# Performance work log

Measured on AMD Instinct MI355X. Metric: run time of the kernel, lower is better.

Reference implementation:

```python
import jax, jax.numpy as jnp
import numpy as np

D = 256      # input_dim
H = 8        # n_heads
HD = D // H  # head_dim = 32
S = 255      # num variables
S1 = S + 1   # new_seq (CLS + vars)
B = 4


def setup_inputs() -> dict:
    key = jax.random.key(0)
    ks = jax.random.split(key, 16)
    g = lambda k, shp, s=0.05: (jax.random.normal(k, shp, dtype=jnp.float32) * s)
    inp = {
        'desc_embeddings': jax.random.normal(ks[0], (B, S, D), dtype=jnp.float32),
        'name_value_embeddings': jax.random.normal(ks[1], (B, S1, D), dtype=jnp.float32),
        # q/k/v projections (nn.Linear: y = x @ W.T + b)
        'qW': g(ks[2], (D, D)), 'qb': jnp.zeros((D,), jnp.float32),
        'kW': g(ks[3], (D, D)), 'kb': jnp.zeros((D,), jnp.float32),
        'vW': g(ks[4], (D, D)), 'vb': jnp.zeros((D,), jnp.float32),
        # edge_update MLP: Linear(2D->D), LayerNorm(D), ReLU, Linear(D->D)
        'eW1': g(ks[5], (D, 2 * D)), 'eb1': jnp.zeros((D,), jnp.float32),
        'ln_g': jnp.ones((D,), jnp.float32), 'ln_b': jnp.zeros((D,), jnp.float32),
        'eW2': g(ks[6], (D, D)), 'eb2': jnp.zeros((D,), jnp.float32),
        # attn_proj: Linear(3*head_dim -> 1)
        'aW': g(ks[7], (1, 3 * HD)), 'ab': jnp.zeros((1,), jnp.float32),
    }
    return inp


def reference(desc_embeddings, name_value_embeddings, qW, qb, kW, kb, vW, vb,
              eW1, eb1, ln_g, ln_b, eW2, eb2, aW, ab):
    nve, desc = name_value_embeddings, desc_embeddings
    b, s1, _ = nve.shape
    s = s1 - 1

    # structure mask: CLS->Var on, Var->CLS off, Var-Var fully connected (self loops kept)
    new_adj = jnp.zeros((b, s1, s1), jnp.float32)
    new_adj = new_adj.at[:, 1:, 1:].set(1.0)
    new_adj = new_adj.at[:, 0, 1:].set(1.0)

    def lin(x, W, bb):
        return x @ W.T + bb

    q = lin(nve, qW, qb).reshape(b, s1, H, HD).transpose(0, 2, 1, 3)  # [B,H,S1,HD]
    k = lin(nve, kW, kb).reshape(b, s1, H, HD).transpose(0, 2, 1, 3)
    v = lin(nve, vW, vb).reshape(b, s1, H, HD).transpose(0, 2, 1, 3)

    # pairwise edge attributes [B,S1,S1,2D]
    di = jnp.broadcast_to(desc[:, :, None, :], (b, s, s, D))
    dj = jnp.broadcast_to(desc[:, None, :, :], (b, s, s, D))
    var_edge = jnp.concatenate([di, dj], axis=-1)              # [B,S,S,2D]
    cls_edge = jnp.concatenate([desc, desc], axis=-1)          # [B,S,2D]
    ea = jnp.zeros((b, s1, s1, 2 * D), jnp.float32)
    ea = ea.at[:, 1:, 1:].set(var_edge)
    ea = ea.at[:, 0, 1:].set(cls_edge)
    ea = ea.at[:, 1:, 0].set(cls_edge)

    # edge_update MLP (edge_type == 'mlp')
    h = lin(ea, eW1, eb1)
    mu = jnp.mean(h, axis=-1, keepdims=True)
    var = jnp.var(h, axis=-1, keepdims=True)
    h = ln_g * (h - mu) / jnp.sqrt(var + 1e-5) + ln_b
    h = jax.nn.relu(h)
    e = lin(h, eW2, eb2)                                       # [B,S1,S1,D]
    e = e.reshape(b, s1, s1, H, HD).transpose(0, 3, 1, 2, 4)    # [B,H,S1,S1,HD]
    e = e * new_adj[:, None, :, :, None]

    # attn_proj(cat(q_i, k_j, e_ij)) == q_i.wq + k_j.wk + e_ij.we + bias (gat_v1, no nonlinearity)
    wq, wk, we = aW[0, :HD], aW[0, HD:2 * HD], aW[0, 2 * HD:]
    logits = (jnp.einsum('bhid,d->bhi', q, wq)[:, :, :, None]
              + jnp.einsum('bhjd,d->bhj', k, wk)[:, :, None, :]
              + jnp.einsum('bhijd,d->bhij', e, we) + ab[0])    # [B,H,S1,S1]

    logits = logits + (new_adj[:, None] == 0).astype(logits.dtype) * -1e9
    attn = jax.nn.softmax(logits, axis=-1)                      # dropout omitted (eval)
    ctx = jnp.einsum('bhij,bhjd->bhid', attn, v)
    basis_outputs = ctx.transpose(0, 2, 1, 3)                   # [B,S1,H,HD]
    return basis_outputs, attn
```

## Files before the change

### kernel.cpp

```cpp
#include <hip/hip_runtime.h>
#include <math.h>

#define S 255
#define B 4

typedef _Float16 half8 __attribute__((ext_vector_type(8)));
typedef float f32x4 __attribute__((ext_vector_type(4)));

#define WS_APJ   0
#define WS_BPJ   131072
#define WS_VTF   262144
#define WS_AP    393216
#define WS_MFG   654336
#define WS_CONST 656384
#define WS_QLOG  656392
#define WS_KLOG  664584

__device__ __forceinline__ half8 cvt8(float4 a, float4 b) {
    half8 h;
    h[0]=(_Float16)a.x; h[1]=(_Float16)a.y; h[2]=(_Float16)a.z; h[3]=(_Float16)a.w;
    h[4]=(_Float16)b.x; h[5]=(_Float16)b.y; h[6]=(_Float16)b.z; h[7]=(_Float16)b.w;
    return h;
}

__global__ __launch_bounds__(256) void k1(
    const float* __restrict__ desc, const float* __restrict__ nve,
    const float* __restrict__ qW, const float* __restrict__ qb,
    const float* __restrict__ kW, const float* __restrict__ kb,
    const float* __restrict__ vW, const float* __restrict__ vb,
    const float* __restrict__ eW1, const float* __restrict__ eb1,
    const float* __restrict__ eW2, const float* __restrict__ eb2,
    const float* __restrict__ aW, float* __restrict__ ws)
{
    const int blk = blockIdx.x;
    const int tid = threadIdx.x;
    __shared__ _Float16 Af[4096];
    __shared__ _Float16 Bf[4096];
    const int wave = tid >> 6, lane = tid & 63;
    const int m16 = lane & 15, quad = lane >> 4;
    const int sr = tid & 63, sko = (tid >> 6) * 16;
    const half8 z8 = {(_Float16)0,(_Float16)0,(_Float16)0,(_Float16)0,
                      (_Float16)0,(_Float16)0,(_Float16)0,(_Float16)0};

    if (blk < 192) {
        const float *X, *W; int M, wst, wof, jobt, sub = blk;
        if (sub < 64)       { X=nve;  W=vW;  M=1024; wst=256; wof=0;   jobt=0; }
        else if (sub < 128) { X=desc; W=eW1; M=1020; wst=512; wof=0;   jobt=1; sub-=64; }
        else                { X=desc; W=eW1; M=1020; wst=512; wof=256; jobt=2; sub-=128; }
        int mBase = (sub>>2)*64, nBase = (sub&3)*64;
        f32x4 acc[2][2] = {};
        for (int k0 = 0; k0 < 256; k0 += 64) {
            half8 xa[2], wb[2];
            int xr = mBase + sr, wr = nBase + sr;
            #pragma unroll
            for (int hh = 0; hh < 2; hh++) {
                int kk = k0 + sko + hh*8;
                if (xr < M) xa[hh] = cvt8(*(const float4*)&X[xr*256 + kk],
                                          *(const float4*)&X[xr*256 + kk + 4]);
                else xa[hh] = z8;
                wb[hh] = cvt8(*(const float4*)&W[wr*wst + wof + kk],
                              *(const float4*)&W[wr*wst + wof + kk + 4]);
            }
            __syncthreads();
            #pragma unroll
            for (int hh = 0; hh < 2; hh++) {
                int krel = sko + hh*8;
                int c = krel >> 5, q2 = (krel >> 3) & 3;
                int ld = (sr & 15) + 16*q2, rt = sr >> 4;
                *(half8*)&Af[((rt*2 + c)*64 + ld)*8] = xa[hh];
                *(half8*)&Bf[((rt*2 + c)*64 + ld)*8] = wb[hh];
            }
            __syncthreads();
            int rt0 = (wave >> 1)*2, ct0 = (wave & 1)*2;
            #pragma unroll
            for (int c = 0; c < 2; c++) {
                half8 A0 = *(const half8*)&Af[(((rt0    )*2 + c)*64 + lane)*8];
                half8 A1 = *(const half8*)&Af[(((rt0 + 1)*2 + c)*64 + lane)*8];
                half8 B0 = *(const half8*)&Bf[(((ct0    )*2 + c)*64 + lane)*8];
                half8 B1 = *(const half8*)&Bf[(((ct0 + 1)*2 + c)*64 + lane)*8];
                acc[0][0] = __builtin_amdgcn_mfma_f32_16x16x32_f16(A0, B0, acc[0][0], 0,0,0);
                acc[0][1] = __builtin_amdgcn_mfma_f32_16x16x32_f16(A0, B1, acc[0][1], 0,0,0);
                acc[1][0] = __builtin_amdgcn_mfma_f32_16x16x32_f16(A1, B0, acc[1][0], 0,0,0);
                acc[1][1] = __builtin_amdgcn_mfma_f32_16x16x32_f16(A1, B1, acc[1][1], 0,0,0);
            }
        }
        int rt0 = (wave >> 1)*2, ct0 = (wave & 1)*2;
        if (jobt == 0) {
            _Float16* vtf = (_Float16*)(ws + WS_VTF);
            #pragma unroll
            for (int ci = 0; ci < 2; ci++) {
                int col = nBase + (ct0 + ci)*16 + m16;
                float bv = vb[col];
                int ct = col >> 4, n = col & 15;
                #pragma unroll
                for (int ri = 0; ri < 2; ri++)
                    #pragma unroll
                    for (int r = 0; r < 4; r++) {
                        int rr = mBase + (rt0 + ri)*16 + quad*4 + r;
                        int bb = rr >> 8, j = rr & 255;
                        int js = j >> 5, qv = (j >> 3) & 3, ev = j & 7;
                        float o = acc[ri][ci][r] + bv;
                        vtf[bb*65536 + (((ct*8 + js)*64 + n + 16*qv) << 3) + ev] = (_Float16)o;
                    }
            }
        } else {
            _Float16* OJ = (_Float16*)(ws + ((jobt == 1) ? WS_APJ : WS_BPJ));
            #pragma unroll
            for (int ci = 0; ci < 2; ci++) {
                int col = nBase + (ct0 + ci)*16 + m16;
                float bv = (jobt == 1) ? eb1[col] : 0.f;
                int ks = col >> 5, q = (col >> 3) & 3, e = col & 7;
                #pragma unroll
                for (int ri = 0; ri < 2; ri++)
                    #pragma unroll
                    for (int r = 0; r < 4; r++) {
                        int rr = mBase + (rt0 + ri)*16 + quad*4 + r;
                        if (rr < 1020) {
                            float o = acc[ri][ci][r] + bv;
                            int bb = rr / 255;
                            int j = rr - bb*255 + 1;
                            int jt = j >> 4, mm = j & 15;
                            OJ[bb*65536 + (((jt*8 + ks)*64 + mm + 16*q) << 3) + e] = (_Float16)o;
                            if (jobt == 1) ws[WS_AP + rr*256 + col] = o;
                        }
                    }
            }
        }
    } else if (blk < 208) {
        {
            int d = tid;
            float f[16] = {0,0,0,0,0,0,0,0,0,0,0,0,0,0,0,0};
            for (int hd = 0; hd < 32; hd++) {
                float wq = aW[hd], wk = aW[32+hd];
                #pragma unroll
                for (int h = 0; h < 8; h++) {
                    f[h]   = fmaf(wq, qW[(h*32+hd)*256 + d], f[h]);
                    f[8+h] = fmaf(wk, kW[(h*32+hd)*256 + d], f[8+h]);
                }
            }
            int ksd = d >> 5, q2 = (d >> 3) & 3, jj = d & 7;
            #pragma unroll
            for (int n = 0; n < 16; n++)
                Bf[((ksd*64 + n + 16*q2))*8 + jj] = (_Float16)f[n];
        }
        __syncthreads();
        int mBase = (blk - 192)*64;
        f32x4 acc = {0.f,0.f,0.f,0.f};
        for (int k0 = 0; k0 < 256; k0 += 64) {
            half8 xa[2];
            #pragma unroll
            for (int hh = 0; hh < 2; hh++) {
                int kk = k0 + sko + hh*8;
                xa[hh] = cvt8(*(const float4*)&nve[(mBase + sr)*256 + kk],
                              *(const float4*)&nve[(mBase + sr)*256 + kk + 4]);
            }
            __syncthreads();
            #pragma unroll
            for (int hh = 0; hh < 2; hh++) {
                int krel = sko + hh*8;
                int c = krel >> 5, q2 = (krel >> 3) & 3;
                int ld = (sr & 15) + 16*q2, rt = sr >> 4;
                *(half8*)&Af[((rt*2 + c)*64 + ld)*8] = xa[hh];
            }
            __syncthreads();
            #pragma unroll
            for (int c = 0; c < 2; c++) {
                half8 A  = *(const half8*)&Af[((wave*2 + c)*64 + lane)*8];
                half8 Bv = *(const half8*)&Bf[(((k0 >> 5) + c)*64 + lane)*8];
                acc = __builtin_amdgcn_mfma_f32_16x16x32_f16(A, Bv, acc, 0,0,0);
            }
        }
        #pragma unroll
        for (int r = 0; r < 4; r++) {
            int rr = mBase + wave*16 + quad*4 + r;
            int bb = rr >> 8, tt2 = rr & 255;
            if (m16 < 8) ws[WS_QLOG + (bb*8 + m16)*256 + tt2] = acc[r];
            else         ws[WS_KLOG + (bb*8 + m16 - 8)*256 + tt2] = acc[r];
        }
    } else {
        _Float16* mfg = (_Float16*)(ws + WS_MFG);
        int k = tid;
        float a8[8] = {0,0,0,0,0,0,0,0};
        for (int hd = 0; hd < 32; hd++) {
            float we = aW[64+hd];
            #pragma unroll
            for (int h = 0; h < 8; h++)
                a8[h] = fmaf(we, eW2[(h*32+hd)*256 + k], a8[h]);
        }
        int ksd = k >> 5, q2 = (k >> 3) & 3, jj = k & 7;
        #pragma unroll
        for (int h = 0; h < 8; h++)
            mfg[((ksd*64 + h + 16*q2))*8 + jj] = (_Float16)a8[h];
        #pragma unroll
        for (int n = 8; n < 16; n++)
            mfg[((ksd*64 + n + 16*q2))*8 + jj] = (_Float16)0.f;
        {
            _Float16* apj = (_Float16*)(ws + WS_APJ);
            _Float16* bpj = (_Float16*)(ws + WS_BPJ);
            int ks0 = tid >> 5, qz = (tid >> 3) & 3, ez = tid & 7;
            int ad = ((ks0*64 + 16*qz) << 3) + ez;
            #pragma unroll
            for (int bb = 0; bb < 4; bb++) {
                apj[bb*65536 + ad] = (_Float16)0.f;
                bpj[bb*65536 + ad] = (_Float16)0.f;
            }
        }
        if (tid == 0) {
            #pragma unroll
            for (int h = 0; h < 8; h++) {
                float c = 0.f;
                for (int hd = 0; hd < 32; hd++) {
                    c = fmaf(aW[64+hd], eb2[h*32+hd], c);
                    c = fmaf(aW[hd],    qb [h*32+hd], c);
                    c = fmaf(aW[32+hd], kb [h*32+hd], c);
                }
                ws[WS_CONST + h] = c;
            }
        }
    }
}

#define PLS 272

__global__ __launch_bounds__(256, 4) void k3(
    const float* __restrict__ ln_g, const float* __restrict__ ln_b,
    const float* __restrict__ ab, const float* __restrict__ ws,
    float* __restrict__ out)
{
    int b = blockIdx.y, i = blockIdx.x;
    int tid = threadIdx.x;
    __shared__ float klds[2048];
    __shared__ float PL[8*PLS];
    __shared__ float gL[256], bL[256], aL[256];
    __shared__ float2 st[256];
    __shared__ float stG[256], stSB[256], stQB[256], stSA[256], stQA[256];
    __shared__ float baseh[8], mxs[8], sms[8], saqa[8];

    int wave = tid >> 6, lane = tid & 63;
    int m16 = lane & 15, quad = lane >> 4;
    const half8 z8 = {(_Float16)0,(_Float16)0,(_Float16)0,(_Float16)0,
                      (_Float16)0,(_Float16)0,(_Float16)0,(_Float16)0};
    half8 ones8;
    #pragma unroll
    for (int e = 0; e < 8; e++) ones8[e] = (_Float16)1.0f;

    #pragma unroll
    for (int t = 0; t < 8; t++)
        klds[tid + t*256] = ws[WS_KLOG + b*2048 + tid + t*256];
    gL[tid] = ln_g[tid];
    bL[tid] = ln_b[tid];
    float av = (i >= 1) ? ws[WS_AP + ((size_t)(b*S + i - 1))*256 + tid] : 0.f;
    aL[tid] = av;
    {
        float s1 = av, s2 = av*av;
        #pragma unroll
        for (int off = 32; off >= 1; off >>= 1) {
            s1 += __shfl_xor(s1, off, 64);
            s2 += __shfl_xor(s2, off, 64);
        }
        if (lane == 0) { saqa[wave] = s1; saqa[4+wave] = s2; }
    }
    if (tid < 8)
        baseh[tid] = ws[WS_QLOG + (b*8+tid)*256 + i] + ab[0] + ws[WS_CONST + tid];
    __syncthreads();

    const _Float16* mfg = (const _Float16*)(ws + WS_MFG);
    const _Float16* bpj = (const _Float16*)(ws + WS_BPJ) + b*65536;
    const _Float16* apj = (const _Float16*)(ws + WS_APJ) + b*65536;
    const _Float16* vtf = (const _Float16*)(ws + WS_VTF) + b*65536;

    if (i >= 1) {
        #pragma unroll
        for (int tl4 = 0; tl4 < 4; tl4++) {
            int tl = wave*4 + tl4;
            f32x4 accGS = {}, accQB = {};
            #pragma unroll
            for (int ks = 0; ks < 8; ks++) {
                half8 bb = *(const half8*)&bpj[((tl*8+ks)*64 + lane) << 3];
                half8 ags;
                if (m16 == 0)
                    ags = cvt8(*(const float4*)&aL[ks*32 + quad*8],
                               *(const float4*)&aL[ks*32 + quad*8 + 4]);
                else if (m16 == 1) ags = ones8;
                else ags = z8;
                accGS = __builtin_amdgcn_mfma_f32_16x16x32_f16(ags, bb, accGS, 0,0,0);
                accQB = __builtin_amdgcn_mfma_f32_16x16x32_f16(bb,  bb, accQB, 0,0,0);
            }
            int j = tl*16 + m16;
            if (quad == 0) { stG[j] = accGS[0]; stSB[j] = accGS[1]; }
            if (quad == (m16 >> 2)) stQB[j] = accQB[m16 & 3];
        }
    } else {
        #pragma unroll
        for (int tl4 = 0; tl4 < 4; tl4++) {
            int tl = wave*4 + tl4;
            f32x4 accSB = {}, accSA = {}, accG = {}, accQA = {}, accQB = {};
            #pragma unroll
            for (int ks = 0; ks < 8; ks++) {
                int idx = ((tl*8+ks)*64 + lane) << 3;
                half8 bb = *(const half8*)&bpj[idx];
                half8 aa = *(const half8*)&apj[idx];
                half8 a1 = (m16 == 0) ? ones8 : z8;
                accSB = __builtin_amdgcn_mfma_f32_16x16x32_f16(a1, bb, accSB, 0,0,0);
                accSA = __builtin_amdgcn_mfma_f32_16x16x32_f16(a1, aa, accSA, 0,0,0);
                accG  = __builtin_amdgcn_mfma_f32_16x16x32_f16(aa, bb, accG,  0,0,0);
                accQA = __builtin_amdgcn_mfma_f32_16x16x32_f16(aa, aa, accQA, 0,0,0);
                accQB = __builtin_amdgcn_mfma_f32_16x16x32_f16(bb, bb, accQB, 0,0,0);
            }
            int j = tl*16 + m16;
            if (quad == 0) { stSB[j] = accSB[0]; stSA[j] = accSA[0]; }
            if (quad == (m16 >> 2)) {
                int r = m16 & 3;
                stG[j] = accG[r]; stQA[j] = accQA[r]; stQB[j] = accQB[r];
            }
        }
    }
    __syncthreads();

    {
        int j = tid;
        float2 v; v.x = 0.f; v.y = 0.f;
        if (j >= 1) {
            float sa, qa;
            if (i >= 1) {
                sa = saqa[0] + saqa[1] + saqa[2] + saqa[3];
                qa = saqa[4] + saqa[5] + saqa[6] + saqa[7];
            } else {
                sa = stSA[j]; qa = stQA[j];
            }
            float sb = stSB[j], qb2 = stQB[j], g = stG[j];
            float mu  = (sa + sb) * (1.0f/256.0f);
            float var = (qa + qb2 + 2.f*g) * (1.0f/256.0f) - mu*mu;
            float inv = rsqrtf(var + 1e-5f);
            v.x = inv; v.y = -mu*inv;
        }
        st[j] = v;
    }
    __syncthreads();

    f32x4 acc[4] = {};
    float2 sv[4];
    #pragma unroll
    for (int tt = 0; tt < 4; tt++)
        sv[tt] = st[(wave*4 + tt)*16 + m16];

    if (i >= 1) {
        #pragma unroll
        for (int ks = 0; ks < 8; ks++) {
            int k = ks*32 + quad*8;
            float4 a0 = *(const float4*)&aL[k], a1 = *(const float4*)&aL[k+4];
            float4 g0 = *(const float4*)&gL[k], g1 = *(const float4*)&gL[k+4];
            float4 b0 = *(const float4*)&bL[k], b1 = *(const float4*)&bL[k+4];
            half8 bf = *(const half8*)&mfg[(ks*64 + lane) << 3];
            float aa[8] = {a0.x,a0.y,a0.z,a0.w,a1.x,a1.y,a1.z,a1.w};
            float ga[8] = {g0.x,g0.y,g0.z,g0.w,g1.x,g1.y,g1.z,g1.w};
            float be[8] = {b0.x,b0.y,b0.z,b0.w,b1.x,b1.y,b1.z,b1.w};
            #pragma unroll
            for (int tt = 0; tt < 4; tt++) {
                half8 bp = *(const half8*)&bpj[(((wave*4 + tt)*8 + ks)*64 + lane) << 3];
                half8 af;
                #pragma unroll
                for (int e = 0; e < 8; e++) {
                    float c = (float)bp[e] + aa[e];
                    float w = fmaf(fmaf(c, sv[tt].x, sv[tt].y), ga[e], be[e]);
                    af[e] = (_Float16)fmaxf(w, 0.f);
                }
                acc[tt] = __builtin_amdgcn_mfma_f32_16x16x32_f16(af, bf, acc[tt], 0,0,0);
            }
        }
    } else {
        #pragma unroll
        for (int ks = 0; ks < 8; ks++) {
            int k = ks*32 + quad*8;
            float4 g0 = *(const float4*)&gL[k], g1 = *(const float4*)&gL[k+4];
            float4 b0 = *(const float4*)&bL[k], b1 = *(const float4*)&bL[k+4];
            half8 bf = *(const half8*)&mfg[(ks*64 + lane) << 3];
            float ga[8] = {g0.x,g0.y,g0.z,g0.w,g1.x,g1.y,g1.z,g1.w};
            float be[8] = {b0.x,b0.y,b0.z,b0.w,b1.x,b1.y,b1.z,b1.w};
            #pragma unroll
            for (int tt = 0; tt < 4; tt++) {
                int idx = ((((wave*4 + tt)*8 + ks)*64 + lane) << 3);
                half8 bp = *(const half8*)&bpj[idx];
                half8 ap = *(const half8*)&apj[idx];
                half8 af;
                #pragma unroll
                for (int e = 0; e < 8; e++) {
                    float c = (float)ap[e] + (float)bp[e];
                    float w = fmaf(fmaf(c, sv[tt].x, sv[tt].y), ga[e], be[e]);
                    af[e] = (_Float16)fmaxf(w, 0.f);
                }
                acc[tt] = __builtin_amdgcn_mfma_f32_16x16x32_f16(af, bf, acc[tt], 0,0,0);
            }
        }
    }

    if (m16 < 8) {
        float basev = baseh[m16];
        #pragma unroll
        for (int tt = 0; tt < 4; tt++)
            #pragma unroll
            for (int r = 0; r < 4; r++) {
                int jr = (wave*4 + tt)*16 + quad*4 + r;
                float val = basev + klds[m16*256 + jr];
                val += (jr == 0) ? -1e9f : acc[tt][r];
                PL[m16*PLS + jr] = val;
            }
    }
    __syncthreads();

    {
        int h = tid >> 5, sg = tid & 31;
        float mv = -INFINITY;
        #pragma unroll
        for (int r = 0; r < 8; r++) mv = fmaxf(mv, PL[h*PLS + sg + r*32]);
        #pragma unroll
        for (int off = 16; off >= 1; off >>= 1)
            mv = fmaxf(mv, __shfl_xor(mv, off, 64));
        if (sg == 0) mxs[h] = mv;
    }
    __syncthreads();
    float p[8];
    #pragma unroll
    for (int h = 0; h < 8; h++) p[h] = expf(PL[h*PLS + tid] - mxs[h]);
    __syncthreads();
    #pragma unroll
    for (int h = 0; h < 8; h++) PL[h*PLS + tid] = p[h];
    __syncthreads();
    {
        int h = tid >> 5, sg = tid & 31;
        float sv2 = 0.f;
        #pragma unroll
        for (int r = 0; r < 8; r++) sv2 += PL[h*PLS + sg + r*32];
        #pragma unroll
        for (int off = 16; off >= 1; off >>= 1)
            sv2 += __shfl_xor(sv2, off, 64);
        if (sg == 0) sms[h] = sv2;
    }
    __syncthreads();

    float* attnOut = out + 262144;
    #pragma unroll
    for (int h = 0; h < 8; h++)
        attnOut[((b*8+h)*256 + i)*256 + tid] = p[h] / sms[h];

    {
        f32x4 cacc[4] = {};
        int ct0 = wave*4;
        #pragma unroll
        for (int js = 0; js < 8; js++) {
            half8 af;
            if (m16 < 8) {
                float4 p0 = *(const float4*)&PL[m16*PLS + js*32 + quad*8];
                float4 p1 = *(const float4*)&PL[m16*PLS + js*32 + quad*8 + 4];
                af = cvt8(p0, p1);
            } else af = z8;
            #pragma unroll
            for (int cl = 0; cl < 4; cl++) {
                half8 bf = *(const half8*)&vtf[(((ct0+cl)*8 + js)*64 + lane) << 3];
                cacc[cl] = __builtin_amdgcn_mfma_f32_16x16x32_f16(af, bf, cacc[cl], 0,0,0);
            }
        }
        #pragma unroll
        for (int cl = 0; cl < 4; cl++) {
            int ct = ct0 + cl;
            int h = ct >> 1;
            if (quad == (h >> 2)) {
                float rs = 1.0f / sms[h];
                out[(b*256 + i)*256 + ct*16 + m16] = cacc[cl][h & 3] * rs;
            }
        }
    }
}

extern "C" void kernel_launch(void* const* d_in, const int* in_sizes, int n_in,
                              void* d_out, int out_size, void* d_ws, size_t ws_size,
                              hipStream_t stream)
{
    const float* desc = (const float*)d_in[0];
    const float* nve  = (const float*)d_in[1];
    const float* qW   = (const float*)d_in[2];
    const float* qb   = (const float*)d_in[3];
    const float* kW   = (const float*)d_in[4];
    const float* kb   = (const float*)d_in[5];
    const float* vW   = (const float*)d_in[6];
    const float* vb   = (const float*)d_in[7];
    const float* eW1  = (const float*)d_in[8];
    const float* eb1  = (const float*)d_in[9];
    const float* ln_g = (const float*)d_in[10];
    const float* ln_b = (const float*)d_in[11];
    const float* eW2  = (const float*)d_in[12];
    const float* eb2  = (const float*)d_in[13];
    const float* aW   = (const float*)d_in[14];
    const float* ab   = (const float*)d_in[15];
    float* ws  = (float*)d_ws;
    float* out = (float*)d_out;

    k1<<<dim3(209), 256, 0, stream>>>(desc, nve, qW, qb, kW, kb, vW, vb,
                                      eW1, eb1, eW2, eb2, aW, ws);
    k3<<<dim3(256, 4), 256, 0, stream>>>(ln_g, ln_b, ab, ws, out);
}
```

Measured before the change: 135.8 us.

## Precompute LayerNorm stats in new batched MFMA kernel, streamline softmax

Adds a kernel k2 that computes the per-(i,j) LayerNorm mean and inverse-std for all edge pairs as a tiled 16-row MFMA GEMM. Row stats go to a workspace buffer that k3 reads in place of recomputing per-row GEMV-like MFMAs with mostly zero A operands. The softmax in k3 also becomes one wave per two heads using float4 and __expf, which removes several block barriers. The cost is an extra launch and extra workspace traffic of 2 MB.

```diff
diff --git a/kernel.cpp b/kernel.cpp
--- a/kernel.cpp
+++ b/kernel.cpp
@@ -15,6 +15,7 @@
 #define WS_CONST 656384
 #define WS_QLOG  656392
 #define WS_KLOG  664584
+#define WS_ST    673792
 
 __device__ __forceinline__ half8 cvt8(float4 a, float4 b) {
     half8 h;
@@ -220,6 +221,95 @@
     }
 }
 
+__global__ __launch_bounds__(256) void k2(float* __restrict__ ws)
+{
+    const int rt = blockIdx.x, b = blockIdx.y;
+    const int tid = threadIdx.x;
+    const int wave = tid >> 6, lane = tid & 63;
+    const int m16 = lane & 15, quad = lane >> 4;
+    __shared__ float saL[16], qaL[16], qbL[256];
+
+    const _Float16* bpj = (const _Float16*)(ws + WS_BPJ) + b*65536;
+    const _Float16* apj = (const _Float16*)(ws + WS_APJ) + b*65536;
+    float2* ST = (float2*)(ws + WS_ST) + b*65536;
+
+    half8 ones8;
+    #pragma unroll
+    for (int e = 0; e < 8; e++) ones8[e] = (_Float16)1.0f;
+
+    {
+        int i_loc = wave*4;
+        #pragma unroll
+        for (int rr = 0; rr < 4; rr++) {
+            int il = i_loc + rr;
+            int i = rt*16 + il;
+            float s = 0.f, q = 0.f;
+            if (i >= 1) {
+                float4 v = *(const float4*)&ws[WS_AP + ((size_t)(b*S + i - 1))*256 + lane*4];
+                s = v.x + v.y + v.z + v.w;
+                q = v.x*v.x + v.y*v.y + v.z*v.z + v.w*v.w;
+            }
+            #pragma unroll
+            for (int off = 32; off >= 1; off >>= 1) {
+                s += __shfl_xor(s, off, 64);
+                q += __shfl_xor(q, off, 64);
+            }
+            if (lane == 0) { saL[il] = s; qaL[il] = q; }
+        }
+    }
+
+    float sbR[4];
+    #pragma unroll
+    for (int jt4 = 0; jt4 < 4; jt4++) {
+        int jt = wave*4 + jt4;
+        f32x4 accS = {}, accQ = {};
+        #pragma unroll
+        for (int ks = 0; ks < 8; ks++) {
+            half8 bb = *(const half8*)&bpj[((jt*8 + ks)*64 + lane) << 3];
+            accS = __builtin_amdgcn_mfma_f32_16x16x32_f16(ones8, bb, accS, 0,0,0);
+            accQ = __builtin_amdgcn_mfma_f32_16x16x32_f16(bb, bb, accQ, 0,0,0);
+        }
+        sbR[jt4] = accS[0];
+        if (quad == (m16 >> 2)) qbL[jt*16 + m16] = accQ[m16 & 3];
+    }
+    __syncthreads();
+
+    half8 aa[8];
+    #pragma unroll
+    for (int ks = 0; ks < 8; ks++)
+        aa[ks] = *(const half8*)&apj[((rt*8 + ks)*64 + lane) << 3];
+
+    #pragma unroll
+    for (int jt4 = 0; jt4 < 4; jt4++) {
+        int jt = wave*4 + jt4;
+        f32x4 acc = {};
+        #pragma unroll
+        for (int ks = 0; ks < 8; ks++) {
+            half8 bb = *(const half8*)&bpj[((jt*8 + ks)*64 + lane) << 3];
+            acc = __builtin_amdgcn_mfma_f32_16x16x32_f16(aa[ks], bb, acc, 0,0,0);
+        }
+        int j = jt*16 + m16;
+        float sb = sbR[jt4], qbv = qbL[j];
+        #pragma unroll
+        for (int r = 0; r < 4; r++) {
+            int il = quad*4 + r;
+            int i = rt*16 + il;
+            float sa = saL[il], qa = qaL[il];
+            float mu  = (sa + sb) * (1.0f/256.0f);
+            float var = (qa + qbv + 2.f*acc[r]) * (1.0f/256.0f) - mu*mu;
+            float inv = rsqrtf(var + 1e-5f);
+            float2 o;
+            if (j == 0) { o.x = 0.f; o.y = 0.f; }
+            else        { o.x = inv; o.y = -mu*inv; }
+            if (i >= 1) {
+                ST[i*256 + j] = o;
+                if (i == j) ST[j] = o;
+            }
+        }
+    }
+    if (rt == 0 && tid == 0) { float2 z; z.x = 0.f; z.y = 0.f; ST[0] = z; }
+}
+
 #define PLS 272
 
 __global__ __launch_bounds__(256, 4) void k3(
@@ -233,33 +323,20 @@
     __shared__ float PL[8*PLS];
     __shared__ float gL[256], bL[256], aL[256];
     __shared__ float2 st[256];
-    __shared__ float stG[256], stSB[256], stQB[256], stSA[256], stQA[256];
-    __shared__ float baseh[8], mxs[8], sms[8], saqa[8];
+    __shared__ float baseh[8], sms[8];
 
     int wave = tid >> 6, lane = tid & 63;
     int m16 = lane & 15, quad = lane >> 4;
     const half8 z8 = {(_Float16)0,(_Float16)0,(_Float16)0,(_Float16)0,
                       (_Float16)0,(_Float16)0,(_Float16)0,(_Float16)0};
-    half8 ones8;
-    #pragma unroll
-    for (int e = 0; e < 8; e++) ones8[e] = (_Float16)1.0f;
 
     #pragma unroll
     for (int t = 0; t < 8; t++)
         klds[tid + t*256] = ws[WS_KLOG + b*2048 + tid + t*256];
     gL[tid] = ln_g[tid];
     bL[tid] = ln_b[tid];
-    float av = (i >= 1) ? ws[WS_AP + ((size_t)(b*S + i - 1))*256 + tid] : 0.f;
-    aL[tid] = av;
-    {
-        float s1 = av, s2 = av*av;
-        #pragma unroll
-        for (int off = 32; off >= 1; off >>= 1) {
-            s1 += __shfl_xor(s1, off, 64);
-            s2 += __shfl_xor(s2, off, 64);
-        }
-        if (lane == 0) { saqa[wave] = s1; saqa[4+wave] = s2; }
-    }
+    aL[tid] = (i >= 1) ? ws[WS_AP + ((size_t)(b*S + i - 1))*256 + tid] : 0.f;
+    st[tid] = ((const float2*)(ws + WS_ST))[(((size_t)b*256 + i) << 8) + tid];
     if (tid < 8)
         baseh[tid] = ws[WS_QLOG + (b*8+tid)*256 + i] + ab[0] + ws[WS_CONST + tid];
     __syncthreads();
@@ -268,75 +345,6 @@
     const _Float16* bpj = (const _Float16*)(ws + WS_BPJ) + b*65536;
     const _Float16* apj = (const _Float16*)(ws + WS_APJ) + b*65536;
     const _Float16* vtf = (const _Float16*)(ws + WS_VTF) + b*65536;
-
-    if (i >= 1) {
-        #pragma unroll
-        for (int tl4 = 0; tl4 < 4; tl4++) {
-            int tl = wave*4 + tl4;
-            f32x4 accGS = {}, accQB = {};
-            #pragma unroll
-            for (int ks = 0; ks < 8; ks++) {
-                half8 bb = *(const half8*)&bpj[((tl*8+ks)*64 + lane) << 3];
-                half8 ags;
-                if (m16 == 0)
-                    ags = cvt8(*(const float4*)&aL[ks*32 + quad*8],
-                               *(const float4*)&aL[ks*32 + quad*8 + 4]);
-                else if (m16 == 1) ags = ones8;
-                else ags = z8;
-                accGS = __builtin_amdgcn_mfma_f32_16x16x32_f16(ags, bb, accGS, 0,0,0);
-                accQB = __builtin_amdgcn_mfma_f32_16x16x32_f16(bb,  bb, accQB, 0,0,0);
-            }
-            int j = tl*16 + m16;
-            if (quad == 0) { stG[j] = accGS[0]; stSB[j] = accGS[1]; }
-            if (quad == (m16 >> 2)) stQB[j] = accQB[m16 & 3];
-        }
-    } else {
-        #pragma unroll
-        for (int tl4 = 0; tl4 < 4; tl4++) {
-            int tl = wave*4 + tl4;
-            f32x4 accSB = {}, accSA = {}, accG = {}, accQA = {}, accQB = {};
-            #pragma unroll
-            for (int ks = 0; ks < 8; ks++) {
-                int idx = ((tl*8+ks)*64 + lane) << 3;
-                half8 bb = *(const half8*)&bpj[idx];
-                half8 aa = *(const half8*)&apj[idx];
-                half8 a1 = (m16 == 0) ? ones8 : z8;
-                accSB = __builtin_amdgcn_mfma_f32_16x16x32_f16(a1, bb, accSB, 0,0,0);
-                accSA = __builtin_amdgcn_mfma_f32_16x16x32_f16(a1, aa, accSA, 0,0,0);
-                accG  = __builtin_amdgcn_mfma_f32_16x16x32_f16(aa, bb, accG,  0,0,0);
-                accQA = __builtin_amdgcn_mfma_f32_16x16x32_f16(aa, aa, accQA, 0,0,0);
-                accQB = __builtin_amdgcn_mfma_f32_16x16x32_f16(bb, bb, accQB, 0,0,0);
-            }
-            int j = tl*16 + m16;
-            if (quad == 0) { stSB[j] = accSB[0]; stSA[j] = accSA[0]; }
-            if (quad == (m16 >> 2)) {
-                int r = m16 & 3;
-                stG[j] = accG[r]; stQA[j] = accQA[r]; stQB[j] = accQB[r];
-            }
-        }
-    }
-    __syncthreads();
-
-    {
-        int j = tid;
-        float2 v; v.x = 0.f; v.y = 0.f;
-        if (j >= 1) {
-            float sa, qa;
-            if (i >= 1) {
-                sa = saqa[0] + saqa[1] + saqa[2] + saqa[3];
-                qa = saqa[4] + saqa[5] + saqa[6] + saqa[7];
-            } else {
-                sa = stSA[j]; qa = stQA[j];
-            }
-            float sb = stSB[j], qb2 = stQB[j], g = stG[j];
-            float mu  = (sa + sb) * (1.0f/256.0f);
-            float var = (qa + qb2 + 2.f*g) * (1.0f/256.0f) - mu*mu;
-            float inv = rsqrtf(var + 1e-5f);
-            v.x = inv; v.y = -mu*inv;
-        }
-        st[j] = v;
-    }
-    __syncthreads();
 
     f32x4 acc[4] = {};
     float2 sv[4];
@@ -408,40 +416,30 @@
     }
     __syncthreads();
 
-    {
-        int h = tid >> 5, sg = tid & 31;
-        float mv = -INFINITY;
-        #pragma unroll
-        for (int r = 0; r < 8; r++) mv = fmaxf(mv, PL[h*PLS + sg + r*32]);
-        #pragma unroll
-        for (int off = 16; off >= 1; off >>= 1)
+    float* attnOut = out + 262144;
+    #pragma unroll
+    for (int hh = 0; hh < 2; hh++) {
+        int h = wave*2 + hh;
+        float4 v = *(const float4*)&PL[h*PLS + lane*4];
+        float mv = fmaxf(fmaxf(v.x, v.y), fmaxf(v.z, v.w));
+        #pragma unroll
+        for (int off = 32; off >= 1; off >>= 1)
             mv = fmaxf(mv, __shfl_xor(mv, off, 64));
-        if (sg == 0) mxs[h] = mv;
+        float4 p;
+        p.x = __expf(v.x - mv); p.y = __expf(v.y - mv);
+        p.z = __expf(v.z - mv); p.w = __expf(v.w - mv);
+        float s = p.x + p.y + p.z + p.w;
+        #pragma unroll
+        for (int off = 32; off >= 1; off >>= 1)
+            s += __shfl_xor(s, off, 64);
+        *(float4*)&PL[h*PLS + lane*4] = p;
+        if (lane == 0) sms[h] = s;
+        float rs = 1.0f / s;
+        float4 ao;
+        ao.x = p.x*rs; ao.y = p.y*rs; ao.z = p.z*rs; ao.w = p.w*rs;
+        *(float4*)&attnOut[((b*8+h)*256 + i)*256 + lane*4] = ao;
     }
     __syncthreads();
-    float p[8];
-    #pragma unroll
-    for (int h = 0; h < 8; h++) p[h] = expf(PL[h*PLS + tid] - mxs[h]);
-    __syncthreads();
-    #pragma unroll
-    for (int h = 0; h < 8; h++) PL[h*PLS + tid] = p[h];
-    __syncthreads();
-    {
-        int h = tid >> 5, sg = tid & 31;
-        float sv2 = 0.f;
-        #pragma unroll
-        for (int r = 0; r < 8; r++) sv2 += PL[h*PLS + sg + r*32];
-        #pragma unroll
-        for (int off = 16; off >= 1; off >>= 1)
-            sv2 += __shfl_xor(sv2, off, 64);
-        if (sg == 0) sms[h] = sv2;
-    }
-    __syncthreads();
-
-    float* attnOut = out + 262144;
-    #pragma unroll
-    for (int h = 0; h < 8; h++)
-        attnOut[((b*8+h)*256 + i)*256 + tid] = p[h] / sms[h];
 
     {
         f32x4 cacc[4] = {};
@@ -497,5 +495,6 @@
 
     k1<<<dim3(209), 256, 0, stream>>>(desc, nve, qW, qb, kW, kb, vW, vb,
                                       eW1, eb1, eW2, eb2, aW, ws);
+    k2<<<dim3(16, 4), 256, 0, stream>>>(ws);
     k3<<<dim3(256, 4), 256, 0, stream>>>(ln_g, ln_b, ab, ws, out);
 }
```

New measurement: 141.6 us. +4.2%, slower.

## Process two query rows per block in k3 to reuse edge-MLP operands

Applied to the files above, without the earlier changes.

Each k3 block now handles two query rows (i0, i1) with 512 threads, so the bpj, mfg and vtf fragments are loaded once and fed to MFMAs for both rows. This halves the grid and amortises global and LDS loads. Softmax is rewritten to one wave per (row, head) with float4 loads, shuffle reductions and fast __expf, which cuts the number of block barriers. The per-head constant in k1 is computed with a parallel shuffle reduction instead of a single thread. In exchange the block uses more LDS and registers, which may lower occupancy, and the special CLS-row handling becomes more complex.

```diff
diff --git a/kernel.cpp b/kernel.cpp
--- a/kernel.cpp
+++ b/kernel.cpp
@@ -15,6 +15,8 @@
 #define WS_CONST 656384
 #define WS_QLOG  656392
 #define WS_KLOG  664584
+
+#define PLS 272
 
 __device__ __forceinline__ half8 cvt8(float4 a, float4 b) {
     half8 h;
@@ -205,39 +207,36 @@
                 bpj[bb*65536 + ad] = (_Float16)0.f;
             }
         }
-        if (tid == 0) {
-            #pragma unroll
-            for (int h = 0; h < 8; h++) {
-                float c = 0.f;
-                for (int hd = 0; hd < 32; hd++) {
-                    c = fmaf(aW[64+hd], eb2[h*32+hd], c);
-                    c = fmaf(aW[hd],    qb [h*32+hd], c);
-                    c = fmaf(aW[32+hd], kb [h*32+hd], c);
-                }
-                ws[WS_CONST + h] = c;
-            }
+        {
+            int h = tid >> 5, hd = tid & 31;
+            float c = aW[64+hd]*eb2[h*32+hd] + aW[hd]*qb[h*32+hd] + aW[32+hd]*kb[h*32+hd];
+            #pragma unroll
+            for (int off = 16; off >= 1; off >>= 1)
+                c += __shfl_xor(c, off, 32);
+            if (hd == 0) ws[WS_CONST + h] = c;
         }
     }
 }
 
-#define PLS 272
-
-__global__ __launch_bounds__(256, 4) void k3(
+__global__ __launch_bounds__(512, 4) void k3(
     const float* __restrict__ ln_g, const float* __restrict__ ln_b,
     const float* __restrict__ ab, const float* __restrict__ ws,
     float* __restrict__ out)
 {
-    int b = blockIdx.y, i = blockIdx.x;
-    int tid = threadIdx.x;
+    const int b = blockIdx.y, gx = blockIdx.x;
+    const int i0 = gx*2, i1 = gx*2 + 1;
+    const int tid = threadIdx.x;
+    const int wave = tid >> 6, lane = tid & 63;
+    const int m16 = lane & 15, quad = lane >> 4;
+    const bool sp = (gx == 0);
+
     __shared__ float klds[2048];
-    __shared__ float PL[8*PLS];
-    __shared__ float gL[256], bL[256], aL[256];
-    __shared__ float2 st[256];
-    __shared__ float stG[256], stSB[256], stQB[256], stSA[256], stQA[256];
-    __shared__ float baseh[8], mxs[8], sms[8], saqa[8];
-
-    int wave = tid >> 6, lane = tid & 63;
-    int m16 = lane & 15, quad = lane >> 4;
+    __shared__ float PL0[8*PLS], PL1[8*PLS];
+    __shared__ float gL[256], bL[256], aL0[256], aL1[256];
+    __shared__ float2 st0[256], st1[256];
+    __shared__ float stG0[256], stG1[256], stSB[256], stQB[256], stSA[256], stQA[256];
+    __shared__ float baseh[16], sms[16], saqa[16];
+
     const half8 z8 = {(_Float16)0,(_Float16)0,(_Float16)0,(_Float16)0,
                       (_Float16)0,(_Float16)0,(_Float16)0,(_Float16)0};
     half8 ones8;
@@ -245,23 +244,27 @@
     for (int e = 0; e < 8; e++) ones8[e] = (_Float16)1.0f;
 
     #pragma unroll
-    for (int t = 0; t < 8; t++)
-        klds[tid + t*256] = ws[WS_KLOG + b*2048 + tid + t*256];
-    gL[tid] = ln_g[tid];
-    bL[tid] = ln_b[tid];
-    float av = (i >= 1) ? ws[WS_AP + ((size_t)(b*S + i - 1))*256 + tid] : 0.f;
-    aL[tid] = av;
+    for (int t = 0; t < 4; t++)
+        klds[tid + t*512] = ws[WS_KLOG + b*2048 + tid + t*512];
+    if (tid < 256) { gL[tid] = ln_g[tid]; bL[tid] = ln_b[tid]; }
     {
+        int hf = tid >> 8, t8 = tid & 255;
+        int ih = hf ? i1 : i0;
+        float av = (ih >= 1) ? ws[WS_AP + ((size_t)(b*S + ih - 1))*256 + t8] : 0.f;
+        (hf ? aL1 : aL0)[t8] = av;
         float s1 = av, s2 = av*av;
         #pragma unroll
         for (int off = 32; off >= 1; off >>= 1) {
             s1 += __shfl_xor(s1, off, 64);
             s2 += __shfl_xor(s2, off, 64);
         }
-        if (lane == 0) { saqa[wave] = s1; saqa[4+wave] = s2; }
-    }
-    if (tid < 8)
-        baseh[tid] = ws[WS_QLOG + (b*8+tid)*256 + i] + ab[0] + ws[WS_CONST + tid];
+        int hw = wave >> 2, sub = wave & 3;
+        if (lane == 0) { saqa[hw*8 + sub] = s1; saqa[hw*8 + 4 + sub] = s2; }
+    }
+    if (tid < 16) {
+        int h = tid & 7, ih = (tid >> 3) ? i1 : i0;
+        baseh[tid] = ws[WS_QLOG + (b*8+h)*256 + ih] + ab[0] + ws[WS_CONST + h];
+    }
     __syncthreads();
 
     const _Float16* mfg = (const _Float16*)(ws + WS_MFG);
@@ -269,204 +272,198 @@
     const _Float16* apj = (const _Float16*)(ws + WS_APJ) + b*65536;
     const _Float16* vtf = (const _Float16*)(ws + WS_VTF) + b*65536;
 
-    if (i >= 1) {
-        #pragma unroll
-        for (int tl4 = 0; tl4 < 4; tl4++) {
-            int tl = wave*4 + tl4;
+    if (!sp) {
+        #pragma unroll
+        for (int t2 = 0; t2 < 2; t2++) {
+            int tl = wave*2 + t2;
             f32x4 accGS = {}, accQB = {};
             #pragma unroll
             for (int ks = 0; ks < 8; ks++) {
                 half8 bb = *(const half8*)&bpj[((tl*8+ks)*64 + lane) << 3];
                 half8 ags;
                 if (m16 == 0)
-                    ags = cvt8(*(const float4*)&aL[ks*32 + quad*8],
-                               *(const float4*)&aL[ks*32 + quad*8 + 4]);
-                else if (m16 == 1) ags = ones8;
+                    ags = cvt8(*(const float4*)&aL0[ks*32 + quad*8],
+                               *(const float4*)&aL0[ks*32 + quad*8 + 4]);
+                else if (m16 == 1)
+                    ags = cvt8(*(const float4*)&aL1[ks*32 + quad*8],
+                               *(const float4*)&aL1[ks*32 + quad*8 + 4]);
+                else if (m16 == 2) ags = ones8;
                 else ags = z8;
                 accGS = __builtin_amdgcn_mfma_f32_16x16x32_f16(ags, bb, accGS, 0,0,0);
                 accQB = __builtin_amdgcn_mfma_f32_16x16x32_f16(bb,  bb, accQB, 0,0,0);
             }
             int j = tl*16 + m16;
-            if (quad == 0) { stG[j] = accGS[0]; stSB[j] = accGS[1]; }
+            if (quad == 0) { stG0[j] = accGS[0]; stG1[j] = accGS[1]; stSB[j] = accGS[2]; }
             if (quad == (m16 >> 2)) stQB[j] = accQB[m16 & 3];
         }
     } else {
         #pragma unroll
-        for (int tl4 = 0; tl4 < 4; tl4++) {
-            int tl = wave*4 + tl4;
-            f32x4 accSB = {}, accSA = {}, accG = {}, accQA = {}, accQB = {};
+        for (int t2 = 0; t2 < 2; t2++) {
+            int tl = wave*2 + t2;
+            f32x4 accSB = {}, accSA = {}, accG = {}, accQA = {}, accQB = {}, accG1 = {};
             #pragma unroll
             for (int ks = 0; ks < 8; ks++) {
                 int idx = ((tl*8+ks)*64 + lane) << 3;
                 half8 bb = *(const half8*)&bpj[idx];
                 half8 aa = *(const half8*)&apj[idx];
                 half8 a1 = (m16 == 0) ? ones8 : z8;
+                half8 ag1;
+                if (m16 == 0)
+                    ag1 = cvt8(*(const float4*)&aL1[ks*32 + quad*8],
+                               *(const float4*)&aL1[ks*32 + quad*8 + 4]);
+                else ag1 = z8;
                 accSB = __builtin_amdgcn_mfma_f32_16x16x32_f16(a1, bb, accSB, 0,0,0);
                 accSA = __builtin_amdgcn_mfma_f32_16x16x32_f16(a1, aa, accSA, 0,0,0);
                 accG  = __builtin_amdgcn_mfma_f32_16x16x32_f16(aa, bb, accG,  0,0,0);
                 accQA = __builtin_amdgcn_mfma_f32_16x16x32_f16(aa, aa, accQA, 0,0,0);
                 accQB = __builtin_amdgcn_mfma_f32_16x16x32_f16(bb, bb, accQB, 0,0,0);
+                accG1 = __builtin_amdgcn_mfma_f32_16x16x32_f16(ag1, bb, accG1, 0,0,0);
             }
             int j = tl*16 + m16;
-            if (quad == 0) { stSB[j] = accSB[0]; stSA[j] = accSA[0]; }
+            if (quad == 0) { stSB[j] = accSB[0]; stSA[j] = accSA[0]; stG1[j] = accG1[0]; }
             if (quad == (m16 >> 2)) {
                 int r = m16 & 3;
-                stG[j] = accG[r]; stQA[j] = accQA[r]; stQB[j] = accQB[r];
+                stG0[j] = accG[r]; stQA[j] = accQA[r]; stQB[j] = accQB[r];
             }
         }
     }
     __syncthreads();
 
     {
-        int j = tid;
+        int hf = tid >> 8, j = tid & 255;
         float2 v; v.x = 0.f; v.y = 0.f;
         if (j >= 1) {
             float sa, qa;
-            if (i >= 1) {
-                sa = saqa[0] + saqa[1] + saqa[2] + saqa[3];
-                qa = saqa[4] + saqa[5] + saqa[6] + saqa[7];
-            } else {
-                sa = stSA[j]; qa = stQA[j];
-            }
-            float sb = stSB[j], qb2 = stQB[j], g = stG[j];
+            if (sp && hf == 0) { sa = stSA[j]; qa = stQA[j]; }
+            else {
+                int base = hf ? 8 : 0;
+                sa = saqa[base+0] + saqa[base+1] + saqa[base+2] + saqa[base+3];
+                qa = saqa[base+4] + saqa[base+5] + saqa[base+6] + saqa[base+7];
+            }
+            float g = hf ? stG1[j] : stG0[j];
+            float sb = stSB[j], qb2 = stQB[j];
             float mu  = (sa + sb) * (1.0f/256.0f);
             float var = (qa + qb2 + 2.f*g) * (1.0f/256.0f) - mu*mu;
             float inv = rsqrtf(var + 1e-5f);
             v.x = inv; v.y = -mu*inv;
         }
-        st[j] = v;
+        (hf ? st1 : st0)[j] = v;
     }
     __syncthreads();
 
-    f32x4 acc[4] = {};
-    float2 sv[4];
+    f32x4 acc[2][2] = {};
+    float2 sv0[2], sv1[2];
     #pragma unroll
-    for (int tt = 0; tt < 4; tt++)
-        sv[tt] = st[(wave*4 + tt)*16 + m16];
-
-    if (i >= 1) {
-        #pragma unroll
-        for (int ks = 0; ks < 8; ks++) {
-            int k = ks*32 + quad*8;
-            float4 a0 = *(const float4*)&aL[k], a1 = *(const float4*)&aL[k+4];
-            float4 g0 = *(const float4*)&gL[k], g1 = *(const float4*)&gL[k+4];
-            float4 b0 = *(const float4*)&bL[k], b1 = *(const float4*)&bL[k+4];
-            half8 bf = *(const half8*)&mfg[(ks*64 + lane) << 3];
-            float aa[8] = {a0.x,a0.y,a0.z,a0.w,a1.x,a1.y,a1.z,a1.w};
-            float ga[8] = {g0.x,g0.y,g0.z,g0.w,g1.x,g1.y,g1.z,g1.w};
-            float be[8] = {b0.x,b0.y,b0.z,b0.w,b1.x,b1.y,b1.z,b1.w};
-            #pragma unroll
-            for (int tt = 0; tt < 4; tt++) {
-                half8 bp = *(const half8*)&bpj[(((wave*4 + tt)*8 + ks)*64 + lane) << 3];
-                half8 af;
-                #pragma unroll
-                for (int e = 0; e < 8; e++) {
-                    float c = (float)bp[e] + aa[e];
-                    float w = fmaf(fmaf(c, sv[tt].x, sv[tt].y), ga[e], be[e]);
-                    af[e] = (_Float16)fmaxf(w, 0.f);
-                }
-                acc[tt] = __builtin_amdgcn_mfma_f32_16x16x32_f16(af, bf, acc[tt], 0,0,0);
-            }
-        }
-    } else {
-        #pragma unroll
-        for (int ks = 0; ks < 8; ks++) {
-            int k = ks*32 + quad*8;
-            float4 g0 = *(const float4*)&gL[k], g1 = *(const float4*)&gL[k+4];
-            float4 b0 = *(const float4*)&bL[k], b1 = *(const float4*)&bL[k+4];
-            half8 bf = *(const half8*)&mfg[(ks*64 + lane) << 3];
-            float ga[8] = {g0.x,g0.y,g0.z,g0.w,g1.x,g1.y,g1.z,g1.w};
-            float be[8] = {b0.x,b0.y,b0.z,b0.w,b1.x,b1.y,b1.z,b1.w};
-            #pragma unroll
-            for (int tt = 0; tt < 4; tt++) {
-                int idx = ((((wave*4 + tt)*8 + ks)*64 + lane) << 3);
-                half8 bp = *(const half8*)&bpj[idx];
-                half8 ap = *(const half8*)&apj[idx];
-                half8 af;
-                #pragma unroll
-                for (int e = 0; e < 8; e++) {
-                    float c = (float)ap[e] + (float)bp[e];
-                    float w = fmaf(fmaf(c, sv[tt].x, sv[tt].y), ga[e], be[e]);
-                    af[e] = (_Float16)fmaxf(w, 0.f);
-                }
-                acc[tt] = __builtin_amdgcn_mfma_f32_16x16x32_f16(af, bf, acc[tt], 0,0,0);
-            }
+    for (int tt = 0; tt < 2; tt++) {
+        sv0[tt] = st0[(wave*2 + tt)*16 + m16];
+        sv1[tt] = st1[(wave*2 + tt)*16 + m16];
+    }
+
+    #pragma unroll
+    for (int ks = 0; ks < 8; ks++) {
+        int k = ks*32 + quad*8;
+        float4 a00 = *(const float4*)&aL0[k], a01 = *(const float4*)&aL0[k+4];
+        float4 a10 = *(const float4*)&aL1[k], a11 = *(const float4*)&aL1[k+4];
+        float4 g0 = *(const float4*)&gL[k], g1 = *(const float4*)&gL[k+4];
+        float4 b0 = *(const float4*)&bL[k], b1 = *(const float4*)&bL[k+4];
+        half8 bf = *(const half8*)&mfg[(ks*64 + lane) << 3];
+        float aa0[8] = {a00.x,a00.y,a00.z,a00.w,a01.x,a01.y,a01.z,a01.w};
+        float aa1[8] = {a10.x,a10.y,a10.z,a10.w,a11.x,a11.y,a11.z,a11.w};
+        float ga[8] = {g0.x,g0.y,g0.z,g0.w,g1.x,g1.y,g1.z,g1.w};
+        float be[8] = {b0.x,b0.y,b0.z,b0.w,b1.x,b1.y,b1.z,b1.w};
+        #pragma unroll
+        for (int tt = 0; tt < 2; tt++) {
+            int idx2 = ((((wave*2 + tt)*8 + ks)*64 + lane) << 3);
+            half8 bp = *(const half8*)&bpj[idx2];
+            half8 app = sp ? *(const half8*)&apj[idx2] : z8;
+            half8 af0, af1;
+            #pragma unroll
+            for (int e = 0; e < 8; e++) {
+                float bpe = (float)bp[e];
+                float c0 = (sp ? (float)app[e] : aa0[e]) + bpe;
+                float w0 = fmaf(fmaf(c0, sv0[tt].x, sv0[tt].y), ga[e], be[e]);
+                af0[e] = (_Float16)fmaxf(w0, 0.f);
+                float c1 = aa1[e] + bpe;
+                float w1 = fmaf(fmaf(c1, sv1[tt].x, sv1[tt].y), ga[e], be[e]);
+                af1[e] = (_Float16)fmaxf(w1, 0.f);
+            }
+            acc[0][tt] = __builtin_amdgcn_mfma_f32_16x16x32_f16(af0, bf, acc[0][tt], 0,0,0);
+            acc[1][tt] = __builtin_amdgcn_mfma_f32_16x16x32_f16(af1, bf, acc[1][tt], 0,0,0);
         }
     }
 
     if (m16 < 8) {
-        float basev = baseh[m16];
-        #pragma unroll
-        for (int tt = 0; tt < 4; tt++)
+        float basev0 = baseh[m16], basev1 = baseh[8 + m16];
+        #pragma unroll
+        for (int tt = 0; tt < 2; tt++)
             #pragma unroll
             for (int r = 0; r < 4; r++) {
-                int jr = (wave*4 + tt)*16 + quad*4 + r;
-                float val = basev + klds[m16*256 + jr];
-                val += (jr == 0) ? -1e9f : acc[tt][r];
-                PL[m16*PLS + jr] = val;
-            }
-    }
-    __syncthreads();
-
-    {
-        int h = tid >> 5, sg = tid & 31;
-        float mv = -INFINITY;
-        #pragma unroll
-        for (int r = 0; r < 8; r++) mv = fmaxf(mv, PL[h*PLS + sg + r*32]);
-        #pragma unroll
-        for (int off = 16; off >= 1; off >>= 1)
-            mv = fmaxf(mv, __shfl_xor(mv, off, 64));
-        if (sg == 0) mxs[h] = mv;
-    }
-    __syncthreads();
-    float p[8];
-    #pragma unroll
-    for (int h = 0; h < 8; h++) p[h] = expf(PL[h*PLS + tid] - mxs[h]);
-    __syncthreads();
-    #pragma unroll
-    for (int h = 0; h < 8; h++) PL[h*PLS + tid] = p[h];
-    __syncthreads();
-    {
-        int h = tid >> 5, sg = tid & 31;
-        float sv2 = 0.f;
-        #pragma unroll
-        for (int r = 0; r < 8; r++) sv2 += PL[h*PLS + sg + r*32];
-        #pragma unroll
-        for (int off = 16; off >= 1; off >>= 1)
-            sv2 += __shfl_xor(sv2, off, 64);
-        if (sg == 0) sms[h] = sv2;
+                int jr = (wave*2 + tt)*16 + quad*4 + r;
+                float kv = klds[m16*256 + jr];
+                float v0 = basev0 + kv + ((jr == 0) ? -1e9f : acc[0][tt][r]);
+                float v1 = basev1 + kv + ((jr == 0) ? -1e9f : acc[1][tt][r]);
+                PL0[m16*PLS + jr] = v0;
+                PL1[m16*PLS + jr] = v1;
+            }
     }
     __syncthreads();
 
     float* attnOut = out + 262144;
     #pragma unroll
-    for (int h = 0; h < 8; h++)
-        attnOut[((b*8+h)*256 + i)*256 + tid] = p[h] / sms[h];
+    for (int hh = 0; hh < 2; hh++) {
+        int row = wave*2 + hh;
+        int ihf = row >> 3, h = row & 7;
+        float* PLp = ihf ? PL1 : PL0;
+        int iv = ihf ? i1 : i0;
+        float4 v = *(const float4*)&PLp[h*PLS + lane*4];
+        float mv = fmaxf(fmaxf(v.x, v.y), fmaxf(v.z, v.w));
+        #pragma unroll
+        for (int off = 32; off >= 1; off >>= 1)
+            mv = fmaxf(mv, __shfl_xor(mv, off, 64));
+        float4 p;
+        p.x = __expf(v.x - mv); p.y = __expf(v.y - mv);
+        p.z = __expf(v.z - mv); p.w = __expf(v.w - mv);
+        float ss = p.x + p.y + p.z + p.w;
+        #pragma unroll
+        for (int off = 32; off >= 1; off >>= 1)
+            ss += __shfl_xor(ss, off, 64);
+        *(float4*)&PLp[h*PLS + lane*4] = p;
+        if (lane == 0) sms[row] = ss;
+        float rs = 1.0f / ss;
+        float4 ao;
+        ao.x = p.x*rs; ao.y = p.y*rs; ao.z = p.z*rs; ao.w = p.w*rs;
+        *(float4*)&attnOut[((b*8+h)*256 + iv)*256 + lane*4] = ao;
+    }
+    __syncthreads();
 
     {
-        f32x4 cacc[4] = {};
-        int ct0 = wave*4;
+        f32x4 cacc[2][2] = {};
+        int ct0 = wave*2;
         #pragma unroll
         for (int js = 0; js < 8; js++) {
-            half8 af;
+            half8 af0, af1;
             if (m16 < 8) {
-                float4 p0 = *(const float4*)&PL[m16*PLS + js*32 + quad*8];
-                float4 p1 = *(const float4*)&PL[m16*PLS + js*32 + quad*8 + 4];
-                af = cvt8(p0, p1);
-            } else af = z8;
-            #pragma unroll
-            for (int cl = 0; cl < 4; cl++) {
+                float4 p00 = *(const float4*)&PL0[m16*PLS + js*32 + quad*8];
+                float4 p01 = *(const float4*)&PL0[m16*PLS + js*32 + quad*8 + 4];
+                af0 = cvt8(p00, p01);
+                float4 p10 = *(const float4*)&PL1[m16*PLS + js*32 + quad*8];
+                float4 p11 = *(const float4*)&PL1[m16*PLS + js*32 + quad*8 + 4];
+                af1 = cvt8(p10, p11);
+            } else { af0 = z8; af1 = z8; }
+            #pragma unroll
+            for (int cl = 0; cl < 2; cl++) {
                 half8 bf = *(const half8*)&vtf[(((ct0+cl)*8 + js)*64 + lane) << 3];
-                cacc[cl] = __builtin_amdgcn_mfma_f32_16x16x32_f16(af, bf, cacc[cl], 0,0,0);
-            }
-        }
-        #pragma unroll
-        for (int cl = 0; cl < 4; cl++) {
+                cacc[0][cl] = __builtin_amdgcn_mfma_f32_16x16x32_f16(af0, bf, cacc[0][cl], 0,0,0);
+                cacc[1][cl] = __builtin_amdgcn_mfma_f32_16x16x32_f16(af1, bf, cacc[1][cl], 0,0,0);
+            }
+        }
+        #pragma unroll
+        for (int cl = 0; cl < 2; cl++) {
             int ct = ct0 + cl;
             int h = ct >> 1;
             if (quad == (h >> 2)) {
-                float rs = 1.0f / sms[h];
-                out[(b*256 + i)*256 + ct*16 + m16] = cacc[cl][h & 3] * rs;
+                out[(b*256 + i0)*256 + ct*16 + m16] = cacc[0][cl][h & 3] * (1.0f / sms[h]);
+                out[(b*256 + i1)*256 + ct*16 + m16] = cacc[1][cl][h & 3] * (1.0f / sms[8 + h]);
             }
         }
     }
@@ -497,5 +494,5 @@
 
     k1<<<dim3(209), 256, 0, stream>>>(desc, nve, qW, qb, kW, kb, vW, vb,
                                       eW1, eb1, eW2, eb2, aW, ws);
-    k3<<<dim3(256, 4), 256, 0, stream>>>(ln_g, ln_b, ab, ws, out);
+    k3<<<dim3(128, 4), 512, 0, stream>>>(ln_g, ln_b, ab, ws, out);
 }
```

Measured after the change: 125.9 us. 1.08x faster.
